# Kernel optimization log

Hardware: AMD Instinct MI355X
Metric: run time of the kernel (lower is better)

## Reference

```python
import jax, jax.numpy as jnp
import numpy as np

B, N, NC = 8, 25200, 80           # YOLOv5-640 / COCO raw output
CONF_THRES = 0.25                  # init conf_threshold
IOU_THRES = 0.45                   # init iou_threshold
PATCH_CONF = 0.001                 # hard-coded patch_conf in forward
GN = jnp.array([640.0, 640.0, 640.0, 640.0], dtype=jnp.float32)  # img_size[[1,0,1,0]]
MAX_WH = 4096.0                    # class offset for class-aware NMS
K_CLEAN = 512                      # fixed-size cap on NMS candidates (clean branch)
K_PATCH = 1024                     # fixed-size cap on NMS candidates (patch branch)
MAX_DET_CLEAN = 1000
MAX_DET_PATCH = 30000
NEG = jnp.float32(-1e30)


def _xywh2xyxy(x):
    xy, wh = x[..., :2], x[..., 2:4]
    return jnp.concatenate([xy - wh * 0.5, xy + wh * 0.5], axis=-1)


def _pairwise_iou(a, b):
    # a: [A,4] xyxy, b: [B,4] xyxy -> [A,B] jaccard overlap
    tl = jnp.maximum(a[:, None, :2], b[None, :, :2])
    br = jnp.minimum(a[:, None, 2:4], b[None, :, 2:4])
    wh = jnp.clip(br - tl, 0.0)
    inter = wh[..., 0] * wh[..., 1]
    area_a = (a[:, 2] - a[:, 0]) * (a[:, 3] - a[:, 1])
    area_b = (b[:, 2] - b[:, 0]) * (b[:, 3] - b[:, 1])
    union = area_a[:, None] + area_b[None, :] - inter
    union = jnp.where(union > 0, union, 1.0)  # guard degenerate boxes
    return inter / union


def _nms_single(pred, conf_thres, K, max_det):
    # pred: [N, 5+nc]. Fixed-size (padded/masked) greedy NMS, class-aware via MAX_WH offset.
    obj = pred[:, 4]
    cls_conf = pred[:, 5:] * obj[:, None]          # x[:,5:] *= x[:,4:5]
    conf = jnp.max(cls_conf, axis=-1)
    cls = jnp.argmax(cls_conf, axis=-1)
    box = _xywh2xyxy(pred[:, :4])
    valid = (obj > conf_thres) & (conf > conf_thres)
    scores = jnp.where(valid, conf, NEG)
    top_scores, idx = jax.lax.top_k(scores, K)     # sorted desc, like torchvision NMS ordering
    boxes = box[idx]
    cls_k = cls[idx]
    valid_k = top_scores > conf_thres
    boxes_off = boxes + cls_k.astype(boxes.dtype)[:, None] * MAX_WH
    iou = jax.lax.stop_gradient(_pairwise_iou(boxes_off, boxes_off))
    ar = jnp.arange(K)

    def step(keep, i):
        sup = keep[i] & (iou[i] > IOU_THRES) & (ar > i)
        return keep & (~sup), None

    keep, _ = jax.lax.scan(step, valid_k, jnp.arange(K))
    rank = jnp.cumsum(keep.astype(jnp.int32))
    keep = keep & (rank <= max_det)
    return boxes, cls_k, keep


def _image_loss(cb, cc, ck, pb, pc, pk):
    # per clean detection: max IoU over kept patch boxes of the same class (0 if none)
    iou = _pairwise_iou(cb / GN, pb / GN)          # [K_CLEAN, K_PATCH]
    mask = ck[:, None] & pk[None, :] & (cc[:, None] == pc[None, :])
    tm = jnp.max(jnp.where(mask, iou, 0.0), axis=1)
    s = jnp.sum(jnp.where(ck, tm, 0.0))
    n = jnp.sum(ck.astype(jnp.float32))
    return s, n


def _forward(output_clean, output_patch):
    cb, cc, ck = jax.vmap(lambda p: _nms_single(p, CONF_THRES, K_CLEAN, MAX_DET_CLEAN))(output_clean)
    pb, pc, pk = jax.vmap(lambda p: _nms_single(p, PATCH_CONF, K_PATCH, MAX_DET_PATCH))(output_patch)
    s, n = jax.vmap(_image_loss)(cb, cc, ck, pb, pc, pk)
    total, cnt = jnp.sum(s), jnp.sum(n)
    return jnp.where(cnt > 0, 1.0 - total / jnp.maximum(cnt, 1.0), jnp.float32(1.0))


def _make_pred(key):
    ka, kb, kc, kd = jax.random.split(key, 4)
    cxcy = jax.random.uniform(ka, (B, N, 2), jnp.float32, 20.0, 620.0)
    wh = jax.random.uniform(kb, (B, N, 2), jnp.float32, 2.0, 150.0)
    obj = jax.random.uniform(kc, (B, N, 1), jnp.float32)
    clsp = jax.random.uniform(kd, (B, N, NC), jnp.float32)
    return jnp.concatenate([cxcy, wh, obj, clsp], axis=-1)


def setup_inputs() -> dict:
    key = jax.random.key(0)
    k1, k2 = jax.random.split(key)
    return {"output_clean": _make_pred(k1), "output_patch": _make_pred(k2)}


def reference(output_clean, output_patch):
    return _forward(output_clean, output_patch)
```

## Files before the change

### kernel.cpp

```cpp
#include <hip/hip_runtime.h>


static constexpr int NB   = 8;
static constexpr int NA   = 25200;
static constexpr int NCLS = 80;
static constexpr int CH   = 85;
static constexpr int NT   = 16;
static constexpr int KMAX = 1024;
static constexpr int NBIN = 32768;
static constexpr int PSH  = 17;
static constexpr int CAP  = 2048;
static constexpr int IOB  = 34;

static constexpr size_t OFF_KEYS = 0;
static constexpr size_t OFF_CLS  = OFF_KEYS + (size_t)NT * NA * 4;
static constexpr size_t OFF_BOX  = OFF_CLS  + (size_t)NT * NA * 4;
static constexpr size_t OFF_CLSK = OFF_BOX  + (size_t)NT * KMAX * 16;
static constexpr size_t OFF_VALK = OFF_CLSK + (size_t)NT * KMAX * 4;
static constexpr size_t OFF_KEEP = OFF_VALK + (size_t)NT * KMAX * 4;
static constexpr size_t OFF_SUP  = OFF_KEEP + (size_t)NT * 16 * 8;
static constexpr size_t OFF_DIAG = OFF_SUP  + (size_t)NT * KMAX * 16 * 8;
static constexpr size_t OFF_PART = OFF_DIAG + (size_t)NT * KMAX * 8;

__device__ __forceinline__ unsigned okey(float f) {
  unsigned u = __float_as_uint(f);
  return (u & 0x80000000u) ? ~u : (u | 0x80000000u);
}

__global__ __launch_bounds__(256) void k_score(const float* __restrict__ clean,
                                               const float* __restrict__ patch,
                                               unsigned* __restrict__ keys,
                                               int* __restrict__ clsArr) {
#pragma clang fp contract(off)
  const int t  = blockIdx.y;
  const int a0 = blockIdx.x * 64;
  const int nA = (NA - a0 < 64) ? (NA - a0) : 64;
  const float conf_th = (t < 8) ? 0.25f : 0.001f;
  const float* __restrict__ src = ((t < 8) ? clean : patch) + (size_t)(t & 7) * NA * CH;
  __shared__ float rows[64 * CH];
  const float4* g4 = (const float4*)(src + (size_t)a0 * CH);
  float4* rows4 = (float4*)rows;
  const int n4 = (nA * CH) >> 2;
  const int wave = threadIdx.x >> 6;
  const int lane = threadIdx.x & 63;
  const int nchunk = (n4 + 63) >> 6;
  for (int c = wave; c < nchunk; c += 4) {
    const int i = (c << 6) + lane;
    if (i < n4) {
      __builtin_amdgcn_global_load_lds(
          (const __attribute__((address_space(1))) void*)(g4 + i),
          (__attribute__((address_space(3))) void*)(rows4 + (c << 6)),
          16, 0, 0);
    }
  }
  __syncthreads();

  const int ar = threadIdx.x >> 2;
  const int q  = threadIdx.x & 3;
  if (ar < nA) {
    const float* r = rows + ar * CH;
    const float obj = r[4];
    const int c0 = q * 20;
    float best = r[5 + c0] * obj;
    int bc = c0;
    for (int c = c0 + 1; c < c0 + 20; ++c) {
      float v = r[5 + c] * obj;
      if (v > best) { best = v; bc = c; }
    }
    {
      float b2 = __shfl_down(best, 2); int c2 = __shfl_down(bc, 2);
      if (b2 > best || (b2 == best && c2 < bc)) { best = b2; bc = c2; }
      float b1 = __shfl_down(best, 1); int c1 = __shfl_down(bc, 1);
      if (b1 > best || (b1 == best && c1 < bc)) { best = b1; bc = c1; }
    }
    if (q == 0) {
      const bool valid = (obj > conf_th) && (best > conf_th);
      const float score = valid ? best : -1e30f;
      const int a = a0 + ar;
      keys[(size_t)t * NA + a]   = okey(score);
      clsArr[(size_t)t * NA + a] = bc;
    }
  }
}

__global__ __launch_bounds__(1024) void k_topsel(const unsigned* __restrict__ keys,
                                                 const int* __restrict__ clsArr,
                                                 const float* __restrict__ clean,
                                                 const float* __restrict__ patch,
                                                 float* __restrict__ boxesK,
                                                 int* __restrict__ clsK,
                                                 int* __restrict__ validK) {
#pragma clang fp contract(off)
  const int t = blockIdx.x;
  const unsigned K = (t < 8) ? 512u : 1024u;
  const float conf_th = (t < 8) ? 0.25f : 0.001f;
  __shared__ unsigned h32[NBIN / 2];
  __shared__ unsigned long long buf[CAP];
  __shared__ unsigned scnt[2];
  __shared__ unsigned wtot[16], wsuf[16];
  __shared__ int s_chunk;
  __shared__ unsigned s_acc, s_B;
  const int tid = threadIdx.x;
  const int lane = tid & 63, wv = tid >> 6;
  for (int i = tid; i < NBIN / 2; i += 1024) h32[i] = 0u;
  for (int i = tid; i < CAP; i += 1024) buf[i] = 0ull;
  if (tid < 2) scnt[tid] = 0u;
  __syncthreads();
  const unsigned INVKEY = okey(-1e30f);
  const unsigned* kv = keys + (size_t)t * NA;
  for (int i = tid; i < 25600; i += 1024) {
    const bool inb = (i < NA);
    unsigned key = inb ? kv[i] : 0u;
    const bool inv = inb && (key == INVKEY);
    unsigned long long mb = __ballot(inv);
    if (inb && !inv) {
      unsigned b = key >> PSH;
      atomicAdd(&h32[b >> 1], 1u << ((b & 1) * 16));
    } else if (inv && lane == (int)__ffsll(mb) - 1) {
      unsigned b = INVKEY >> PSH;
      atomicAdd(&h32[b >> 1], (unsigned)__popcll(mb) << ((b & 1) * 16));
    }
  }
  __syncthreads();
  unsigned cnt_c = 0;
  for (int i = 0; i < 16; ++i) {
    unsigned v = h32[tid * 16 + i];
    cnt_c += (v & 0xFFFFu) + (v >> 16);
  }
  unsigned s = cnt_c;
  for (int off = 1; off < 64; off <<= 1) {
    unsigned v = __shfl_down(s, off);
    if (lane + off < 64) s += v;
  }
  if (lane == 0) wtot[wv] = s;
  __syncthreads();
  if (tid < 16) {
    unsigned acc = 0;
    for (int w2 = 15; w2 > tid; --w2) acc += wtot[w2];
    wsuf[tid] = acc;
  }
  __syncthreads();
  const unsigned suf = s + wsuf[wv];
  if (suf >= K && suf - cnt_c < K) { s_chunk = tid; s_acc = suf - cnt_c; }
  __syncthreads();
  if (tid == 0) {
    unsigned acc = s_acc;
    unsigned res = (unsigned)(s_chunk * 32);
    for (int i = 31; i >= 0; --i) {
      int bb = s_chunk * 32 + i;
      unsigned v = h32[bb >> 1];
      unsigned c2 = (bb & 1) ? (v >> 16) : (v & 0xFFFFu);
      if (acc + c2 >= K) { res = (unsigned)bb; break; }
      acc += c2;
    }
    s_B = res;
  }
  __syncthreads();
  const unsigned B = s_B;
  const unsigned long long lowmask =
      (lane == 0) ? 0ull : (0xFFFFFFFFFFFFFFFFull >> (64 - lane));
  for (int i = tid; i < 25600; i += 1024) {
    const bool inb = (i < NA);
    unsigned key = inb ? kv[i] : 0u;
    unsigned p = key >> PSH;
    const bool hi = inb && (p > B);
    const bool eq = inb && (p == B);
    const unsigned long long item =
        ((unsigned long long)key << 32) | (unsigned)(~(unsigned)i);
    unsigned long long mh = __ballot(hi);
    if (mh) {
      int leader = (int)__ffsll(mh) - 1;
      unsigned base2 = 0;
      if (lane == leader) base2 = atomicAdd(&scnt[0], (unsigned)__popcll(mh));
      base2 = __shfl(base2, leader);
      if (hi) {
        unsigned pos = base2 + (unsigned)__popcll(mh & lowmask);
        if (pos < 1024u) buf[pos] = item;
      }
    }
    unsigned long long me = __ballot(eq);
    if (me) {
      int leader = (int)__ffsll(me) - 1;
      unsigned base2 = 0;
      if (lane == leader) base2 = atomicAdd(&scnt[1], (unsigned)__popcll(me));
      base2 = __shfl(base2, leader);
      if (eq) {
        unsigned pos = base2 + (unsigned)__popcll(me & lowmask);
        if (pos < 1024u) buf[1024 + pos] = item;
      }
    }
  }
  __syncthreads();
  for (int kk2 = 2; kk2 <= CAP; kk2 <<= 1) {
    for (int j = kk2 >> 1; j > 0; j >>= 1) {
      for (int i = tid; i < CAP; i += 1024) {
        int ixj = i ^ j;
        if (ixj > i) {
          unsigned long long a = buf[i], b = buf[ixj];
          bool desc = ((i & kk2) == 0);
          if (desc ? (a < b) : (a > b)) { buf[i] = b; buf[ixj] = a; }
        }
      }
      __syncthreads();
    }
  }
  const float* __restrict__ src = ((t < 8) ? clean : patch) + (size_t)(t & 7) * NA * CH;
  const unsigned vkey = okey(conf_th);
  for (int k = tid; k < (int)K; k += 1024) {
    unsigned long long v = buf[k];
    unsigned key = (unsigned)(v >> 32);
    int idx = (int)(~(unsigned)(v & 0xFFFFFFFFull));
    if (idx < 0 || idx >= NA) idx = 0;
    const float* r = src + (size_t)idx * CH;
    float cx = r[0], cy = r[1], w = r[2], h = r[3];
    float hw = w * 0.5f, hh = h * 0.5f;
    float* bo = boxesK + ((size_t)t * KMAX + k) * 4;
    bo[0] = cx - hw; bo[1] = cy - hh; bo[2] = cx + hw; bo[3] = cy + hh;
    clsK[t * KMAX + k]   = clsArr[(size_t)t * NA + idx];
    validK[t * KMAX + k] = (key > vkey) ? 1 : 0;
  }
}

__global__ __launch_bounds__(256) void k_ioumat(const float* __restrict__ boxesK,
                                                const int* __restrict__ clsK,
                                                unsigned long long* __restrict__ sup,
                                                unsigned long long* __restrict__ diag) {
#pragma clang fp contract(off)
  const int t  = blockIdx.y;
  const int K  = (t < 8) ? 512 : 1024;
  const int lw = (t < 8) ? 3 : 4;
  const int nw = 1 << lw;
  const int npair = (nw * (nw + 1)) / 2;
  const int total = npair * 64;
  if (blockIdx.x * 256 >= total) return;
  __shared__ float X1[KMAX + 16], Y1[KMAX + 16], X2[KMAX + 16], Y2[KMAX + 16], AR[KMAX + 16];
  for (int i = threadIdx.x; i < K; i += 256) {
    const float* bo = boxesK + ((size_t)t * KMAX + i) * 4;
    float off = (float)clsK[t * KMAX + i] * 4096.0f;
    float x1 = bo[0] + off, y1 = bo[1] + off, x2 = bo[2] + off, y2 = bo[3] + off;
    const int ip = i + (i >> 6);
    X1[ip] = x1; Y1[ip] = y1; X2[ip] = x2; Y2[ip] = y2;
    AR[ip] = (x2 - x1) * (y2 - y1);
  }
  __syncthreads();
  unsigned long long* supt = sup + (size_t)t * (KMAX * 16);
  for (int widx = blockIdx.x * 256 + threadIdx.x; widx < total; widx += IOB * 256) {
    int p = widx >> 6;
    int row = widx & 63;
    int rb = 0, pr = p;
    while (pr >= nw - rb) { pr -= nw - rb; ++rb; }
    const int wc = rb + pr;
    const int i = rb * 64 + row;
    const int ipi = i + rb;
    const float x1i = X1[ipi], y1i = Y1[ipi], x2i = X2[ipi], y2i = Y2[ipi], ai = AR[ipi];
    unsigned long long m = 0ull;
    const int jb = (wc << 6) + wc;
    const bool offd = (wc > rb);
#pragma unroll 4
    for (int l = 0; l < 64; ++l) {
      const int jp = jb + l;
      float tlx = fmaxf(x1i, X1[jp]);
      float tly = fmaxf(y1i, Y1[jp]);
      float brx = fminf(x2i, X2[jp]);
      float bry = fminf(y2i, Y2[jp]);
      float w = fmaxf(brx - tlx, 0.0f);
      float h = fmaxf(bry - tly, 0.0f);
      float inter = w * h;
      float uni = (ai + AR[jp]) - inter;
      uni = (uni > 0.0f) ? uni : 1.0f;
      float iou = inter / uni;
      bool hit = (iou > 0.45f) && (offd || ((wc << 6) + l > i));
      m |= hit ? (1ull << l) : 0ull;
    }
    supt[(size_t)i * nw + wc] = m;
    if (wc == rb) diag[(size_t)t * KMAX + i] = m;
  }
}

__global__ __launch_bounds__(64) void k_greedy(const unsigned long long* __restrict__ sup,
                                               const unsigned long long* __restrict__ diag,
                                               const int* __restrict__ validK,
                                               unsigned long long* __restrict__ keepw) {
  const int t  = blockIdx.x;
  const int K  = (t < 8) ? 512 : 1024;
  const int lw = (t < 8) ? 3 : 4;
  const int nw = 1 << lw;
  const int lane = threadIdx.x;
  __shared__ unsigned long long sdiag[KMAX];
  const unsigned long long* dg = diag + (size_t)t * KMAX;
  for (int i = lane; i < K; i += 64) sdiag[i] = dg[i];
  int v16[16];
#pragma unroll
  for (int W = 0; W < 16; ++W)
    v16[W] = (W < nw) ? validK[t * KMAX + W * 64 + lane] : 0;
  unsigned long long vkeep = 0ull;
#pragma unroll
  for (int W = 0; W < 16; ++W)
    if (W < nw) {
      unsigned long long bl = __ballot(v16[W] != 0);
      if (lane == W) vkeep = bl;
    }
  __syncthreads();
  const int w = lane & (nw - 1);
  const int b = lane >> lw;
  const unsigned long long* base = sup + (size_t)t * (KMAX * 16);
  unsigned long long remv = 0ull;
  for (int W = 0; W < nw; ++W) {
    unsigned long long cur = __shfl(vkeep, W) & ~__shfl(remv, W);
    for (int rb = 0; rb < 64; rb += 16) {
      unsigned long long tm[16];
#pragma unroll
      for (int i2 = 0; i2 < 16; ++i2) tm[i2] = sdiag[W * 64 + rb + i2];
#pragma unroll
      for (int i2 = 0; i2 < 16; ++i2) {
        unsigned long long msk = 0ull - ((cur >> (rb + i2)) & 1ull);
        cur &= ~(tm[i2] & msk);
      }
    }
    if (lane == 0) keepw[t * 16 + W] = cur;
    if (W + 1 < nw) {
      const int r0 = b * nw;
      unsigned long long vv[16];
#pragma unroll
      for (int j = 0; j < 16; ++j) {
        bool take = (j < nw) && (w > W) && ((cur >> (r0 + j)) & 1ull);
        vv[j] = take ? base[(size_t)(W * 64 + r0 + j) * nw + w] : 0ull;
      }
      unsigned long long part = 0ull;
#pragma unroll
      for (int j = 0; j < 16; ++j) part |= vv[j];
      for (int s = nw; s < 64; s <<= 1) part |= __shfl_xor(part, s);
      remv |= part;
    }
  }
}

__global__ __launch_bounds__(1024) void k_loss(const float* __restrict__ boxesK,
                                               const int* __restrict__ clsK,
                                               const unsigned long long* __restrict__ keepw,
                                               float* __restrict__ part) {
#pragma clang fp contract(off)
  const int img = blockIdx.y;
  const int chunk = blockIdx.x;
  const int tp = 8 + img;
  __shared__ float px1[KMAX], py1[KMAX], px2[KMAX], py2[KMAX], pa[KMAX];
  __shared__ int pcls[KMAX];
  __shared__ float red[1024];
  for (int j = threadIdx.x; j < KMAX; j += 1024) {
    const float* bo = boxesK + ((size_t)tp * KMAX + j) * 4;
    float x1 = bo[0] / 640.0f, y1 = bo[1] / 640.0f;
    float x2 = bo[2] / 640.0f, y2 = bo[3] / 640.0f;
    px1[j] = x1; py1[j] = y1; px2[j] = x2; py2[j] = y2;
    pa[j] = (x2 - x1) * (y2 - y1);
    int kept = (int)((keepw[tp * 16 + (j >> 6)] >> (j & 63)) & 1ull);
    pcls[j] = kept ? clsK[tp * KMAX + j] : -1;
  }
  __syncthreads();
  const int row = chunk * 64 + (threadIdx.x & 63);
  const int stripe = threadIdx.x >> 6;
  const int ck = (int)((keepw[img * 16 + (row >> 6)] >> (row & 63)) & 1ull);
  const float* bo = boxesK + ((size_t)img * KMAX + row) * 4;
  float cx1 = bo[0] / 640.0f, cy1 = bo[1] / 640.0f;
  float cx2 = bo[2] / 640.0f, cy2 = bo[3] / 640.0f;
  float ca = (cx2 - cx1) * (cy2 - cy1);
  const int ccls = clsK[img * KMAX + row];
  float m = 0.0f;
  if (ck) {
    const int j0 = stripe * 64;
    for (int j = j0; j < j0 + 64; ++j) {
      if (pcls[j] == ccls) {
        float tlx = fmaxf(cx1, px1[j]);
        float tly = fmaxf(cy1, py1[j]);
        float brx = fminf(cx2, px2[j]);
        float bry = fminf(cy2, py2[j]);
        float w = fmaxf(brx - tlx, 0.0f);
        float h = fmaxf(bry - tly, 0.0f);
        float inter = w * h;
        float uni = (ca + pa[j]) - inter;
        uni = (uni > 0.0f) ? uni : 1.0f;
        m = fmaxf(m, inter / uni);
      }
    }
  }
  red[threadIdx.x] = m;
  __syncthreads();
  if (threadIdx.x < 64) {
    float mm = red[threadIdx.x];
#pragma unroll
    for (int s = 1; s < 16; ++s) mm = fmaxf(mm, red[threadIdx.x + 64 * s]);
    float sv = ck ? mm : 0.0f;
    float nv = ck ? 1.0f : 0.0f;
    for (int off = 32; off > 0; off >>= 1) {
      sv += __shfl_down(sv, off);
      nv += __shfl_down(nv, off);
    }
    if (threadIdx.x == 0) {
      int b = img * 8 + chunk;
      part[b * 2 + 0] = sv;
      part[b * 2 + 1] = nv;
    }
  }
}

__global__ __launch_bounds__(64) void k_final(const float* __restrict__ part,
                                              float* __restrict__ out) {
  int lane = threadIdx.x;
  float sv = part[lane * 2 + 0];
  float nv = part[lane * 2 + 1];
  for (int off = 32; off > 0; off >>= 1) {
    sv += __shfl_down(sv, off);
    nv += __shfl_down(nv, off);
  }
  if (lane == 0) out[0] = (nv > 0.0f) ? (1.0f - sv / fmaxf(nv, 1.0f)) : 1.0f;
}

extern "C" void kernel_launch(void* const* d_in, const int* in_sizes, int n_in,
                              void* d_out, int out_size, void* d_ws, size_t ws_size,
                              hipStream_t stream) {
  const float* clean = (const float*)d_in[0];
  const float* patch = (const float*)d_in[1];
  char* ws = (char*)d_ws;
  unsigned* keys            = (unsigned*)(ws + OFF_KEYS);
  int* clsArr               = (int*)(ws + OFF_CLS);
  float* boxesK             = (float*)(ws + OFF_BOX);
  int* clsK                 = (int*)(ws + OFF_CLSK);
  int* validK               = (int*)(ws + OFF_VALK);
  unsigned long long* keepw = (unsigned long long*)(ws + OFF_KEEP);
  unsigned long long* sup   = (unsigned long long*)(ws + OFF_SUP);
  unsigned long long* diag  = (unsigned long long*)(ws + OFF_DIAG);
  float* part               = (float*)(ws + OFF_PART);
  float* out                = (float*)d_out;

  k_score  <<<dim3((NA + 63) / 64, NT), 256, 0, stream>>>(clean, patch, keys, clsArr);
  k_topsel <<<NT, 1024, 0, stream>>>(keys, clsArr, clean, patch, boxesK, clsK, validK);
  k_ioumat <<<dim3(IOB, NT), 256, 0, stream>>>(boxesK, clsK, sup, diag);
  k_greedy <<<NT, 64, 0, stream>>>(sup, diag, validK, keepw);
  k_loss   <<<dim3(8, NB), 1024, 0, stream>>>(boxesK, clsK, keepw, part);
  k_final  <<<1, 64, 0, stream>>>(part, out);
}
```

Measured before the change: 274.7 us.

## Register-resident bitonic sort with wave shuffles and vectorized histogram key loads

Replaces the shared-memory bitonic sort of the 2048 candidate keys with a register version. Each thread holds two elements, strides below 64 use cross-lane xor shuffles, stride 64 is an in-thread compare, and only strides of 128 or more go through shared memory with barriers. This removes most __syncthreads and LDS traffic from the top-K select stage. The histogram pass also loads keys as uint4 and counts invalid keys per thread with a wave reduction instead of per-iteration ballots, which adds a small cost for the extra register shuffles.

```diff
diff --git a/kernel.cpp b/kernel.cpp
--- a/kernel.cpp
+++ b/kernel.cpp
@@ -25,6 +25,13 @@
 __device__ __forceinline__ unsigned okey(float f) {
   unsigned u = __float_as_uint(f);
   return (u & 0x80000000u) ? ~u : (u | 0x80000000u);
+}
+
+__device__ __forceinline__ unsigned long long shflx64(unsigned long long v, int m) {
+  unsigned lo = (unsigned)v, hi = (unsigned)(v >> 32);
+  lo = __shfl_xor(lo, m);
+  hi = __shfl_xor(hi, m);
+  return ((unsigned long long)hi << 32) | lo;
 }
 
 __global__ __launch_bounds__(256) void k_score(const float* __restrict__ clean,
@@ -108,17 +115,26 @@
   __syncthreads();
   const unsigned INVKEY = okey(-1e30f);
   const unsigned* kv = keys + (size_t)t * NA;
-  for (int i = tid; i < 25600; i += 1024) {
-    const bool inb = (i < NA);
-    unsigned key = inb ? kv[i] : 0u;
-    const bool inv = inb && (key == INVKEY);
-    unsigned long long mb = __ballot(inv);
-    if (inb && !inv) {
-      unsigned b = key >> PSH;
-      atomicAdd(&h32[b >> 1], 1u << ((b & 1) * 16));
-    } else if (inv && lane == (int)__ffsll(mb) - 1) {
+  {
+    const uint4* kv4 = (const uint4*)kv;
+    unsigned invCnt = 0;
+    for (int i = tid; i < NA / 4; i += 1024) {
+      uint4 kq = kv4[i];
+      unsigned kk[4] = {kq.x, kq.y, kq.z, kq.w};
+#pragma unroll
+      for (int c = 0; c < 4; ++c) {
+        if (kk[c] == INVKEY) {
+          ++invCnt;
+        } else {
+          unsigned b = kk[c] >> PSH;
+          atomicAdd(&h32[b >> 1], 1u << ((b & 1) * 16));
+        }
+      }
+    }
+    for (int off = 32; off > 0; off >>= 1) invCnt += __shfl_down(invCnt, off);
+    if (lane == 0 && invCnt) {
       unsigned b = INVKEY >> PSH;
-      atomicAdd(&h32[b >> 1], (unsigned)__popcll(mb) << ((b & 1) * 16));
+      atomicAdd(&h32[b >> 1], invCnt << ((b & 1) * 16));
     }
   }
   __syncthreads();
@@ -191,19 +207,42 @@
     }
   }
   __syncthreads();
-  for (int kk2 = 2; kk2 <= CAP; kk2 <<= 1) {
-    for (int j = kk2 >> 1; j > 0; j >>= 1) {
-      for (int i = tid; i < CAP; i += 1024) {
-        int ixj = i ^ j;
-        if (ixj > i) {
-          unsigned long long a = buf[i], b = buf[ixj];
-          bool desc = ((i & kk2) == 0);
-          if (desc ? (a < b) : (a > b)) { buf[i] = b; buf[ixj] = a; }
+  {
+    const int e0 = wv * 128 + lane;
+    const int e1 = e0 + 64;
+    unsigned long long r0 = buf[e0], r1 = buf[e1];
+    for (int kk2 = 2; kk2 <= CAP; kk2 <<= 1) {
+      for (int j = kk2 >> 1; j > 0; j >>= 1) {
+        if (j >= 128) {
+          buf[e0] = r0; buf[e1] = r1;
+          __syncthreads();
+          unsigned long long o0 = buf[e0 ^ j];
+          unsigned long long o1 = buf[e1 ^ j];
+          const bool mx = (((e0 & kk2) == 0) == ((e0 & j) == 0));
+          r0 = mx ? (r0 > o0 ? r0 : o0) : (r0 < o0 ? r0 : o0);
+          r1 = mx ? (r1 > o1 ? r1 : o1) : (r1 < o1 ? r1 : o1);
+          __syncthreads();
+        } else if (j == 64) {
+          const bool up = (e0 & kk2) == 0;
+          unsigned long long mxv = r0 > r1 ? r0 : r1;
+          unsigned long long mnv = r0 > r1 ? r1 : r0;
+          r0 = up ? mxv : mnv;
+          r1 = up ? mnv : mxv;
+        } else {
+          unsigned long long o0 = shflx64(r0, j);
+          unsigned long long o1 = shflx64(r1, j);
+          const bool up0 = (e0 & kk2) == 0;
+          const bool up1 = (e1 & kk2) == 0;
+          const bool lo  = (lane & j) == 0;
+          const bool m0 = (up0 == lo), m1 = (up1 == lo);
+          r0 = m0 ? (r0 > o0 ? r0 : o0) : (r0 < o0 ? r0 : o0);
+          r1 = m1 ? (r1 > o1 ? r1 : o1) : (r1 < o1 ? r1 : o1);
         }
       }
-      __syncthreads();
-    }
-  }
+    }
+    buf[e0] = r0; buf[e1] = r1;
+  }
+  __syncthreads();
   const float* __restrict__ src = ((t < 8) ? clean : patch) + (size_t)(t & 7) * NA * CH;
   const unsigned vkey = okey(conf_th);
   for (int k = tid; k < (int)K; k += 1024) {
```

New measurement: 258.1 us. -6.0%, faster.
